# Kernel optimization log

Measured on AMD Instinct MI355X. Metric: run time of the kernel, lower is better.

The kernel has to match this reference:

```python
import jax, jax.numpy as jnp
import numpy as np

N = 50000
E = 800000
HID = 128


def _gat_conv(x, src, dst, W, al, ar, b, n):
    # DGL GATConv, num_heads=1, negative_slope=0.2, bias=True
    z = x @ W                                  # [N, F]
    el = z @ al                                # [N]
    er = z @ ar                                # [N]
    e = jax.nn.leaky_relu(el[src] + er[dst], 0.2)   # [E]
    m = jax.ops.segment_max(e, dst, num_segments=n)  # per-dst max for stable softmax
    ex = jnp.exp(e - m[dst])
    denom = jax.ops.segment_sum(ex, dst, num_segments=n)
    alpha = ex / (denom[dst] + 1e-9)           # edge softmax over incoming edges
    out = jax.ops.segment_sum(alpha[:, None] * z[src], dst, num_segments=n)
    return out + b


def setup_inputs() -> dict:
    key = jax.random.key(0)
    ks = jax.random.split(key, 16)
    inp = {
        "x": jax.random.normal(ks[0], (N, 2), jnp.float32),
        "src": jax.random.randint(ks[1], (E,), 0, N, jnp.int32),
        "dst": jax.random.randint(ks[2], (E,), 0, N, jnp.int32),
        "W1": jax.random.normal(ks[3], (2, HID), jnp.float32) * 0.5,
        "al1": jax.random.normal(ks[4], (HID,), jnp.float32) * 0.1,
        "ar1": jax.random.normal(ks[5], (HID,), jnp.float32) * 0.1,
        "b1": jnp.zeros((HID,), jnp.float32),
        "W2": jax.random.normal(ks[6], (HID, HID), jnp.float32) * (1.0 / np.sqrt(HID)),
        "al2": jax.random.normal(ks[7], (HID,), jnp.float32) * 0.1,
        "ar2": jax.random.normal(ks[8], (HID,), jnp.float32) * 0.1,
        "b2": jnp.zeros((HID,), jnp.float32),
        "Wlin": jax.random.normal(ks[9], (HID, 3), jnp.float32) * (1.0 / np.sqrt(HID)),
        "blin": jnp.zeros((3,), jnp.float32),
        "alpha0": jnp.float32(1.0),
        "beta0": jnp.float32(1.0),
        "gamma0": jnp.float32(1.0),
        "dt": jnp.float32(0.5),
    }
    return inp


def reference(x, src, dst, W1, al1, ar1, b1, W2, al2, ar2, b2, Wlin, blin,
              alpha0, beta0, gamma0, dt):
    h = _gat_conv(x, src, dst, W1, al1, ar1, b1, N)
    h = jax.nn.relu(h)
    h = _gat_conv(h, src, dst, W2, al2, ar2, b2, N)
    h = jax.nn.relu(h)
    h = jax.nn.sigmoid(h @ Wlin + blin)        # [N, 3]
    # (original computes unsplice/splice predictions from alpha0/beta0/gamma0/dt
    #  but does not return them; returned value is the mean over rate channels)
    return h.mean(axis=-1)                     # [N]


if __name__ == "__main__":
    out = reference(**setup_inputs())
    print(out.shape, out.dtype)
```

## Files before the change

### kernel.cpp

```cpp
#include <hip/hip_runtime.h>
#include <math.h>

#define NN 50000
#define EE 800000
#define HIDF 128
#define NPAD 50176

#define BSHIFT 9
#define BKTN 98
#define BCAP 10000

typedef unsigned int uint;
typedef unsigned short ushort;
typedef unsigned char uchar;
typedef short bf16x8 __attribute__((ext_vector_type(8)));
typedef float f32x4 __attribute__((ext_vector_type(4)));
typedef float f32x2 __attribute__((ext_vector_type(2)));

__device__ inline ushort bf16_rtne(float x) {
  uint u = __float_as_uint(x);
  return (ushort)((u + 0x7fffu + ((u >> 16) & 1u)) >> 16);
}
__device__ inline uint pack2_bf16(float a, float b) {
  return (uint)bf16_rtne(a) | ((uint)bf16_rtne(b) << 16);
}
__device__ inline float rdlanef(float p, int jj) {
  return __uint_as_float(__builtin_amdgcn_readlane(__float_as_uint(p), jj));
}
__device__ inline float lo16(uint z) { return __uint_as_float(z << 16); }
__device__ inline float hi16(uint z) { return __uint_as_float(z & 0xffff0000u); }

__global__ void k_prep(const float* __restrict__ x, const float* __restrict__ W1,
                       const float* __restrict__ al1, const float* __restrict__ ar1,
                       const float* __restrict__ W2, const float* __restrict__ al2,
                       const float* __restrict__ ar2,
                       ushort* __restrict__ z, float* __restrict__ el, float* __restrict__ er,
                       ushort* __restrict__ Bfrag, float* __restrict__ wel,
                       float* __restrict__ wer, int* __restrict__ bcnt) {
  int b = blockIdx.x, tid = threadIdx.x;
  if (b < 16) {
    int e = b * 1024 + tid * 4;
#pragma unroll
    for (int q = 0; q < 4; ++q, ++e) {
      int k = e >> 7, n = e & 127;
      float v = W2[e];
      ushort hi = bf16_rtne(v);
      ushort lo = bf16_rtne(v - __uint_as_float((uint)hi << 16));
      int g = n >> 4, t = k >> 5;
      int l = (n & 15) | (((k >> 3) & 3) << 4);
      int j = k & 7;
      int idx = ((g * 4 + t) * 64 + l) * 8 + j;
      Bfrag[idx] = hi;
      Bfrag[16384 + idx] = lo;
    }
  } else if (b == 16) {
    if (tid < BKTN) bcnt[tid] = 0;
    if (tid < 128) {
      float acc = 0.f;
      for (int k = 0; k < 128; ++k) acc += W2[k * 128 + tid] * al2[k];
      wel[tid] = acc;
    } else {
      int n = tid - 128;
      float acc = 0.f;
      for (int k = 0; k < 128; ++k) acc += W2[k * 128 + n] * ar2[k];
      wer[n] = acc;
    }
  } else {
    int v = (b - 17) * 4 + (tid >> 6);
    if (v >= NN) return;
    int lane = tid & 63;
    float x0 = x[v * 2 + 0];
    float x1 = x[v * 2 + 1];
    int f0 = lane * 2, f1 = f0 + 1;
    float z0 = fmaf(x0, W1[f0], x1 * W1[HIDF + f0]);
    float z1v = fmaf(x0, W1[f1], x1 * W1[HIDF + f1]);
    ((uint*)(z + (size_t)v * HIDF))[lane] = pack2_bf16(z0, z1v);
    float elp = z0 * al1[f0] + z1v * al1[f1];
    float erp = z0 * ar1[f0] + z1v * ar1[f1];
    for (int o = 32; o; o >>= 1) {
      elp += __shfl_xor(elp, o);
      erp += __shfl_xor(erp, o);
    }
    if (lane == 0) { el[v] = elp; er[v] = erp; }
  }
}

__global__ __launch_bounds__(256) void k_binA(const int* __restrict__ src,
                                              const int* __restrict__ dst,
                                              int* __restrict__ bcnt, uint* __restrict__ bcoo) {
  __shared__ uint stage[4096];
  __shared__ uchar stageb[4096];
  __shared__ int bh[BKTN], bbase[BKTN], gbase[BKTN], lcur[BKTN];
  __shared__ int sc[128];
  int tid = threadIdx.x;
  int e0 = blockIdx.x * 4096;
  int nE = min(4096, EE - e0);
  if (tid < BKTN) bh[tid] = 0;
  __syncthreads();

  int myb[16];
  uint myv[16];
#pragma unroll
  for (int k = 0; k < 16; ++k) {
    int i = e0 + k * 256 + tid;
    myb[k] = -1;
    if (i < EE) {
      int s = src[i], d = dst[i];
      myb[k] = d >> BSHIFT;
      myv[k] = ((uint)s << BSHIFT) | (uint)(d & 511);
      atomicAdd(&bh[myb[k]], 1);
    }
  }
  __syncthreads();

  {
    int v = (tid < BKTN) ? bh[tid] : 0;
    if (tid < 128) sc[tid] = v;
    __syncthreads();
    for (int o = 1; o < 128; o <<= 1) {
      int add = (tid >= o && tid < 128) ? sc[tid - o] : 0;
      __syncthreads();
      if (tid < 128) sc[tid] += add;
      __syncthreads();
    }
    if (tid < BKTN) {
      int excl = sc[tid] - bh[tid];
      bbase[tid] = excl;
      lcur[tid] = excl;
      gbase[tid] = atomicAdd(&bcnt[tid], bh[tid]);
    }
  }
  __syncthreads();

#pragma unroll
  for (int k = 0; k < 16; ++k) {
    if (myb[k] >= 0) {
      int slot = atomicAdd(&lcur[myb[k]], 1);
      stage[slot] = myv[k];
      stageb[slot] = (uchar)myb[k];
    }
  }
  __syncthreads();

  for (int s2 = tid; s2 < nE; s2 += 256) {
    int b = stageb[s2];
    bcoo[(size_t)b * BCAP + gbase[b] + (s2 - bbase[b])] = stage[s2];
  }
}

__global__ __launch_bounds__(256) void k_binB(const uint* __restrict__ bcoo,
                                              const int* __restrict__ bcnt,
                                              int* __restrict__ rowp, int* __restrict__ srcs) {
  __shared__ int h[512], pref[512], ps[256];
  __shared__ int basebuf;
  int b = blockIdx.x, tid = threadIdx.x;
  int cnt = bcnt[b];

  {
    int v = (tid < BKTN) ? bcnt[tid] : 0;
    if (tid < 128) ps[tid] = v;
    __syncthreads();
    for (int o = 1; o < 128; o <<= 1) {
      int add = (tid >= o && tid < 128) ? ps[tid - o] : 0;
      __syncthreads();
      if (tid < 128) ps[tid] += add;
      __syncthreads();
    }
    if (tid == 0) {
      basebuf = (b == 0) ? 0 : ps[b - 1];
      if (b == 0) rowp[NN] = EE;
    }
  }
  h[tid] = 0;
  h[tid + 256] = 0;
  __syncthreads();
  int base = basebuf;
  const uint* mc = bcoo + (size_t)b * BCAP;
  for (int i = tid; i < cnt; i += 256) atomicAdd(&h[mc[i] & 511], 1);
  __syncthreads();
  int a0 = h[2 * tid], a1 = h[2 * tid + 1];
  int s = a0 + a1;
  ps[tid] = s;
  __syncthreads();
  for (int o = 1; o < 256; o <<= 1) {
    int add = (tid >= o) ? ps[tid - o] : 0;
    __syncthreads();
    ps[tid] += add;
    __syncthreads();
  }
  int excl = ps[tid] - s;
  pref[2 * tid] = excl;
  pref[2 * tid + 1] = excl + a0;
  __syncthreads();
  int n0 = b << BSHIFT;
  for (int j = tid; j < 512; j += 256)
    if (n0 + j < NN) rowp[n0 + j] = base + pref[j];
  __syncthreads();
  for (int i = tid; i < cnt; i += 256) {
    uint v = mc[i];
    int pos = atomicAdd(&pref[v & 511], 1);
    srcs[base + pos] = (int)(v >> BSHIFT);
  }
}

__global__ __launch_bounds__(256) void k_gemm_mfma(
    const ushort* __restrict__ Hhi, const ushort* __restrict__ Hlo,
    const ushort* __restrict__ Bfrag, ushort* __restrict__ z) {
  int tid = threadIdx.x;
  int lane = tid & 63;
  int wid = tid >> 6;
  int base = blockIdx.x * 128;

  bf16x8 bhi[2][4], blo[2][4];
  const bf16x8* bp = (const bf16x8*)Bfrag;
#pragma unroll
  for (int gi = 0; gi < 2; ++gi)
#pragma unroll
    for (int t = 0; t < 4; ++t) {
      int idx = ((wid * 2 + gi) * 4 + t) * 64 + lane;
      bhi[gi][t] = bp[idx];
      blo[gi][t] = bp[2048 + idx];
    }

  int arow = lane & 15;
  int koff = (lane >> 4) * 8;
  const bf16x8* ahp = (const bf16x8*)(Hhi + (size_t)(base + arow) * HIDF + koff);
  const bf16x8* alp = (const bf16x8*)(Hlo + (size_t)(base + arow) * HIDF + koff);

  bf16x8 ah[4], av[4];
#pragma unroll
  for (int t = 0; t < 4; ++t) { ah[t] = ahp[t * 4]; av[t] = alp[t * 4]; }

#pragma unroll
  for (int mt = 0; mt < 8; ++mt) {
    bf16x8 nah[4], nav[4];
#pragma unroll
    for (int t = 0; t < 4; ++t) { nah[t] = ah[t]; nav[t] = av[t]; }
    if (mt < 7) {
#pragma unroll
      for (int t = 0; t < 4; ++t) {
        nah[t] = ahp[(mt + 1) * 256 + t * 4];
        nav[t] = alp[(mt + 1) * 256 + t * 4];
      }
    }
    f32x4 c0a = {0.f, 0.f, 0.f, 0.f}, c0b = {0.f, 0.f, 0.f, 0.f};
    f32x4 c1a = {0.f, 0.f, 0.f, 0.f}, c1b = {0.f, 0.f, 0.f, 0.f};
#pragma unroll
    for (int t = 0; t < 4; ++t) {
      f32x4& c0 = (t & 1) ? c0b : c0a;
      f32x4& c1 = (t & 1) ? c1b : c1a;
      c0 = __builtin_amdgcn_mfma_f32_16x16x32_bf16(ah[t], bhi[0][t], c0, 0, 0, 0);
      c1 = __builtin_amdgcn_mfma_f32_16x16x32_bf16(ah[t], bhi[1][t], c1, 0, 0, 0);
      c0 = __builtin_amdgcn_mfma_f32_16x16x32_bf16(ah[t], blo[0][t], c0, 0, 0, 0);
      c1 = __builtin_amdgcn_mfma_f32_16x16x32_bf16(ah[t], blo[1][t], c1, 0, 0, 0);
      c0 = __builtin_amdgcn_mfma_f32_16x16x32_bf16(av[t], bhi[0][t], c0, 0, 0, 0);
      c1 = __builtin_amdgcn_mfma_f32_16x16x32_bf16(av[t], bhi[1][t], c1, 0, 0, 0);
    }
    f32x4 c0 = c0a + c0b;
    f32x4 c1 = c1a + c1b;
    int r0 = base + mt * 16 + (lane >> 4) * 4;
    int cc = wid * 32 + (lane & 15);
    ushort* zp = z + (size_t)r0 * HIDF + cc;
#pragma unroll
    for (int i = 0; i < 4; ++i) {
      zp[i * HIDF] = bf16_rtne(c0[i]);
      zp[i * HIDF + 16] = bf16_rtne(c1[i]);
    }
#pragma unroll
    for (int t = 0; t < 4; ++t) { ah[t] = nah[t]; av[t] = nav[t]; }
  }
}

#define PAIR(JJ)                                                        \
  {                                                                     \
    float pA = rdlanef(p, (JJ)), pB = rdlanef(p, (JJ) + 1);             \
    int sA = __builtin_amdgcn_readlane(s, (JJ));                        \
    int sB = __builtin_amdgcn_readlane(s, (JJ) + 1);                    \
    uint zA = zl[(uint)sA * 64u];                                       \
    uint zB = zl[(uint)sB * 64u];                                       \
    f32x2 vA = {lo16(zA), hi16(zA)};                                    \
    f32x2 vB = {lo16(zB), hi16(zB)};                                    \
    acc = vA * (f32x2){pA, pA} + acc;                                   \
    acc = vB * (f32x2){pB, pB} + acc;                                   \
  }

template <int MODE>
__global__ void k_aggregate(const int* __restrict__ rowp, const int* __restrict__ srcs,
                            const float* __restrict__ el, const float* __restrict__ er,
                            const ushort* __restrict__ z, const float* __restrict__ bias,
                            ushort* __restrict__ Hhi, ushort* __restrict__ Hlo,
                            const float* __restrict__ wel, const float* __restrict__ wer,
                            float* __restrict__ elo, float* __restrict__ ero,
                            float* __restrict__ out,
                            const float* __restrict__ Wlin, const float* __restrict__ blin) {
  int v = blockIdx.x * 4 + (threadIdx.x >> 6);
  if (v >= NN) return;
  int lane = threadIdx.x & 63;
  int beg = rowp[v], end = rowp[v + 1];
  float erv = er[v];
  float psum = 0.f;
  f32x2 acc = {0.f, 0.f};
  const uint* zl = (const uint*)z + lane;

  for (int cb = beg; cb < end; cb += 64) {
    int j = cb + lane;
    int s = srcs[min(j, end - 1)];
    float t = el[s] + erv;
    t = fmaxf(t, 0.2f * t);
    float p = (j < end) ? __expf(t) : 0.f;
    psum += p;
    int cnt = min(64, end - cb);
    int bb = 0;
    for (; bb + 16 <= cnt; bb += 16) {
#pragma unroll
      for (int u = 0; u < 16; u += 2) PAIR(bb + u)
    }
    for (; bb < cnt; bb += 2) PAIR(bb)
  }

  float denom = psum;
  for (int o = 32; o; o >>= 1) denom += __shfl_xor(denom, o);
  float inv = 1.0f / (denom + 1e-9f);
  float2 bv = ((const float2*)bias)[lane];
  float ox = fmaxf(fmaf(acc.x, inv, bv.x), 0.f);
  float oy = fmaxf(fmaf(acc.y, inv, bv.y), 0.f);

  if (MODE == 1) {
    ushort hx = bf16_rtne(ox), hy = bf16_rtne(oy);
    ((uint*)Hhi)[(size_t)v * 64 + lane] = (uint)hx | ((uint)hy << 16);
    float lx = ox - __uint_as_float((uint)hx << 16);
    float ly = oy - __uint_as_float((uint)hy << 16);
    ((uint*)Hlo)[(size_t)v * 64 + lane] = pack2_bf16(lx, ly);
    float2 wl = ((const float2*)wel)[lane];
    float2 wr = ((const float2*)wer)[lane];
    float ep = ox * wl.x + oy * wl.y;
    float rp = ox * wr.x + oy * wr.y;
    for (int o = 32; o; o >>= 1) {
      ep += __shfl_xor(ep, o);
      rp += __shfl_xor(rp, o);
    }
    if (lane == 0) { elo[v] = ep; ero[v] = rp; }
  } else {
    int f0 = lane * 2;
    const float* w0 = &Wlin[f0 * 3];
    float d0 = fmaf(ox, w0[0], oy * w0[3]);
    float d1 = fmaf(ox, w0[1], oy * w0[4]);
    float d2 = fmaf(ox, w0[2], oy * w0[5]);
    for (int o = 32; o; o >>= 1) {
      d0 += __shfl_xor(d0, o);
      d1 += __shfl_xor(d1, o);
      d2 += __shfl_xor(d2, o);
    }
    if (lane == 0) {
      float s0 = 1.f / (1.f + __expf(-(d0 + blin[0])));
      float s1 = 1.f / (1.f + __expf(-(d1 + blin[1])));
      float s2 = 1.f / (1.f + __expf(-(d2 + blin[2])));
      out[v] = (s0 + s1 + s2) * (1.f / 3.f);
    }
  }
}

extern "C" void kernel_launch(void* const* d_in, const int* in_sizes, int n_in,
                              void* d_out, int out_size, void* d_ws, size_t ws_size,
                              hipStream_t stream) {
  const float* x    = (const float*)d_in[0];
  const int*   src  = (const int*)d_in[1];
  const int*   dst  = (const int*)d_in[2];
  const float* W1   = (const float*)d_in[3];
  const float* al1  = (const float*)d_in[4];
  const float* ar1  = (const float*)d_in[5];
  const float* b1   = (const float*)d_in[6];
  const float* W2   = (const float*)d_in[7];
  const float* al2  = (const float*)d_in[8];
  const float* ar2  = (const float*)d_in[9];
  const float* b2   = (const float*)d_in[10];
  const float* Wlin = (const float*)d_in[11];
  const float* blin = (const float*)d_in[12];
  float* out = (float*)d_out;

  char* ws = (char*)d_ws;
  size_t off = 0;
  auto alloc = [&](size_t bytes) -> char* {
    char* p = ws + off;
    off += (bytes + 255) & ~(size_t)255;
    return p;
  };
  int*    rowp    = (int*)alloc((size_t)(NN + 1) * 4);
  int*    srcs    = (int*)alloc((size_t)EE * 4);
  int*    bcnt    = (int*)alloc(BKTN * 4);
  uint*   bcoo    = (uint*)alloc((size_t)BKTN * BCAP * 4);
  float*  el1     = (float*)alloc((size_t)NN * 4);
  float*  er1     = (float*)alloc((size_t)NN * 4);
  float*  el2     = (float*)alloc((size_t)NN * 4);
  float*  er2     = (float*)alloc((size_t)NN * 4);
  float*  wel     = (float*)alloc(HIDF * 4);
  float*  wer     = (float*)alloc(HIDF * 4);
  ushort* Bfrag   = (ushort*)alloc(2 * 16384 * 2);
  ushort* Z       = (ushort*)alloc((size_t)NPAD * HIDF * 2);
  ushort* Hhi     = (ushort*)alloc((size_t)NPAD * HIDF * 2);
  ushort* Hlo     = (ushort*)alloc((size_t)NPAD * HIDF * 2);

  const int nbNode4 = (NN + 3) / 4;
  const int nbGemm = (NN + 127) / 128;
  const int nbBinA = (EE + 4095) / 4096;

  k_prep<<<17 + nbNode4, 256, 0, stream>>>(x, W1, al1, ar1, W2, al2, ar2,
                                           Z, el1, er1, Bfrag, wel, wer, bcnt);

  k_binA<<<nbBinA, 256, 0, stream>>>(src, dst, bcnt, bcoo);
  k_binB<<<BKTN, 256, 0, stream>>>(bcoo, bcnt, rowp, srcs);

  k_aggregate<1><<<nbNode4, 256, 0, stream>>>(rowp, srcs, el1, er1, Z, b1,
                                              Hhi, Hlo, wel, wer, el2, er2,
                                              nullptr, nullptr, nullptr);

  k_gemm_mfma<<<nbGemm, 256, 0, stream>>>(Hhi, Hlo, Bfrag, Z);
  k_aggregate<2><<<nbNode4, 256, 0, stream>>>(rowp, srcs, el2, er2, Z, b2,
                                              nullptr, nullptr, nullptr, nullptr, nullptr, nullptr,
                                              out, Wlin, blin);
}
```

Before: 146.5 us.

## Aggregate layer-1 in 2-D input space instead of 128-wide features

Because layer 1 is linear with a 2-wide input, the attention logits are now computed as x·(W1·al1) and x·(W1·ar1). The softmax-weighted sum aggregates the 2-float x rows rather than the 128-wide bf16 z rows, and W1 and the bias are applied per destination node afterwards. This removes the per-node z/el/er materialisation in k_prep and the 128-feature gather per edge in layer 1. The aggregation is also done per-lane rather than by broadcasting each edge across the wave. The result is now kept in fp32 where it was previously rounded to bf16 z, and the summation order changes.

```diff
diff --git a/kernel.cpp b/kernel.cpp
--- a/kernel.cpp
+++ b/kernel.cpp
@@ -30,13 +30,13 @@
 __device__ inline float lo16(uint z) { return __uint_as_float(z << 16); }
 __device__ inline float hi16(uint z) { return __uint_as_float(z & 0xffff0000u); }
 
-__global__ void k_prep(const float* __restrict__ x, const float* __restrict__ W1,
-                       const float* __restrict__ al1, const float* __restrict__ ar1,
+__global__ void k_prep(const float* __restrict__ W1, const float* __restrict__ al1,
+                       const float* __restrict__ ar1,
                        const float* __restrict__ W2, const float* __restrict__ al2,
                        const float* __restrict__ ar2,
-                       ushort* __restrict__ z, float* __restrict__ el, float* __restrict__ er,
                        ushort* __restrict__ Bfrag, float* __restrict__ wel,
-                       float* __restrict__ wer, int* __restrict__ bcnt) {
+                       float* __restrict__ wer, float* __restrict__ params,
+                       int* __restrict__ bcnt) {
   int b = blockIdx.x, tid = threadIdx.x;
   if (b < 16) {
     int e = b * 1024 + tid * 4;
@@ -53,7 +53,7 @@
       Bfrag[idx] = hi;
       Bfrag[16384 + idx] = lo;
     }
-  } else if (b == 16) {
+  } else {
     if (tid < BKTN) bcnt[tid] = 0;
     if (tid < 128) {
       float acc = 0.f;
@@ -65,23 +65,13 @@
       for (int k = 0; k < 128; ++k) acc += W2[k * 128 + n] * ar2[k];
       wer[n] = acc;
     }
-  } else {
-    int v = (b - 17) * 4 + (tid >> 6);
-    if (v >= NN) return;
-    int lane = tid & 63;
-    float x0 = x[v * 2 + 0];
-    float x1 = x[v * 2 + 1];
-    int f0 = lane * 2, f1 = f0 + 1;
-    float z0 = fmaf(x0, W1[f0], x1 * W1[HIDF + f0]);
-    float z1v = fmaf(x0, W1[f1], x1 * W1[HIDF + f1]);
-    ((uint*)(z + (size_t)v * HIDF))[lane] = pack2_bf16(z0, z1v);
-    float elp = z0 * al1[f0] + z1v * al1[f1];
-    float erp = z0 * ar1[f0] + z1v * ar1[f1];
-    for (int o = 32; o; o >>= 1) {
-      elp += __shfl_xor(elp, o);
-      erp += __shfl_xor(erp, o);
-    }
-    if (lane == 0) { el[v] = elp; er[v] = erp; }
+    if (tid < 4) {
+      const float* vec = (tid & 2) ? ar1 : al1;
+      const float* wrow = W1 + (tid & 1) * HIDF;
+      float acc = 0.f;
+      for (int f = 0; f < HIDF; ++f) acc += wrow[f] * vec[f];
+      params[tid] = acc;
+    }
   }
 }
 
@@ -203,6 +193,62 @@
   }
 }
 
+__global__ void k_agg1(const int* __restrict__ rowp, const int* __restrict__ srcs,
+                       const float* __restrict__ x, const float* __restrict__ params,
+                       const float* __restrict__ W1, const float* __restrict__ b1,
+                       ushort* __restrict__ Hhi, ushort* __restrict__ Hlo,
+                       const float* __restrict__ wel, const float* __restrict__ wer,
+                       float* __restrict__ el2, float* __restrict__ er2) {
+  int v = blockIdx.x * 4 + (threadIdx.x >> 6);
+  if (v >= NN) return;
+  int lane = threadIdx.x & 63;
+  float wl1x = params[0], wl1y = params[1], wr1x = params[2], wr1y = params[3];
+  float2 xv = ((const float2*)x)[v];
+  float erv = fmaf(xv.x, wr1x, xv.y * wr1y);
+  int beg = rowp[v], end = rowp[v + 1];
+
+  float psum = 0.f, ax = 0.f, ay = 0.f;
+  for (int j = beg + lane; j < end; j += 64) {
+    int s = srcs[j];
+    float2 xs = ((const float2*)x)[s];
+    float t = fmaf(xs.x, wl1x, xs.y * wl1y) + erv;
+    t = fmaxf(t, 0.2f * t);
+    float p = __expf(t);
+    psum += p;
+    ax = fmaf(p, xs.x, ax);
+    ay = fmaf(p, xs.y, ay);
+  }
+  for (int o = 32; o; o >>= 1) {
+    psum += __shfl_xor(psum, o);
+    ax += __shfl_xor(ax, o);
+    ay += __shfl_xor(ay, o);
+  }
+  float inv = 1.0f / (psum + 1e-9f);
+  ax *= inv;
+  ay *= inv;
+
+  float2 w0 = ((const float2*)W1)[lane];
+  float2 w1 = ((const float2*)(W1 + HIDF))[lane];
+  float2 bv = ((const float2*)b1)[lane];
+  float ox = fmaxf(fmaf(ax, w0.x, fmaf(ay, w1.x, bv.x)), 0.f);
+  float oy = fmaxf(fmaf(ax, w0.y, fmaf(ay, w1.y, bv.y)), 0.f);
+
+  ushort hx = bf16_rtne(ox), hy = bf16_rtne(oy);
+  ((uint*)Hhi)[(size_t)v * 64 + lane] = (uint)hx | ((uint)hy << 16);
+  float lx = ox - __uint_as_float((uint)hx << 16);
+  float ly = oy - __uint_as_float((uint)hy << 16);
+  ((uint*)Hlo)[(size_t)v * 64 + lane] = pack2_bf16(lx, ly);
+  float2 wl = ((const float2*)wel)[lane];
+  float2 wr = ((const float2*)wer)[lane];
+  float ep = ox * wl.x + oy * wl.y;
+  float rp = ox * wr.x + oy * wr.y;
+  for (int o = 32; o; o >>= 1) {
+    ep += __shfl_xor(ep, o);
+    rp += __shfl_xor(rp, o);
+  }
+  if (lane == 0) { el2[v] = ep; er2[v] = rp; }
+}
+
 __global__ __launch_bounds__(256) void k_gemm_mfma(
     const ushort* __restrict__ Hhi, const ushort* __restrict__ Hlo,
     const ushort* __restrict__ Bfrag, ushort* __restrict__ z) {
@@ -284,15 +330,11 @@
     acc = vB * (f32x2){pB, pB} + acc;                                   \
   }
 
-template <int MODE>
-__global__ void k_aggregate(const int* __restrict__ rowp, const int* __restrict__ srcs,
-                            const float* __restrict__ el, const float* __restrict__ er,
-                            const ushort* __restrict__ z, const float* __restrict__ bias,
-                            ushort* __restrict__ Hhi, ushort* __restrict__ Hlo,
-                            const float* __restrict__ wel, const float* __restrict__ wer,
-                            float* __restrict__ elo, float* __restrict__ ero,
-                            float* __restrict__ out,
-                            const float* __restrict__ Wlin, const float* __restrict__ blin) {
+__global__ void k_agg2(const int* __restrict__ rowp, const int* __restrict__ srcs,
+                       const float* __restrict__ el, const float* __restrict__ er,
+                       const ushort* __restrict__ z, const float* __restrict__ bias,
+                       float* __restrict__ out,
+                       const float* __restrict__ Wlin, const float* __restrict__ blin) {
   int v = blockIdx.x * 4 + (threadIdx.x >> 6);
   if (v >= NN) return;
   int lane = threadIdx.x & 63;
@@ -325,38 +367,21 @@
   float ox = fmaxf(fmaf(acc.x, inv, bv.x), 0.f);
   float oy = fmaxf(fmaf(acc.y, inv, bv.y), 0.f);
 
-  if (MODE == 1) {
-    ushort hx = bf16_rtne(ox), hy = bf16_rtne(oy);
-    ((uint*)Hhi)[(size_t)v * 64 + lane] = (uint)hx | ((uint)hy << 16);
-    float lx = ox - __uint_as_float((uint)hx << 16);
-    float ly = oy - __uint_as_float((uint)hy << 16);
-    ((uint*)Hlo)[(size_t)v * 64 + lane] = pack2_bf16(lx, ly);
-    float2 wl = ((const float2*)wel)[lane];
-    float2 wr = ((const float2*)wer)[lane];
-    float ep = ox * wl.x + oy * wl.y;
-    float rp = ox * wr.x + oy * wr.y;
-    for (int o = 32; o; o >>= 1) {
-      ep += __shfl_xor(ep, o);
-      rp += __shfl_xor(rp, o);
-    }
-    if (lane == 0) { elo[v] = ep; ero[v] = rp; }
-  } else {
-    int f0 = lane * 2;
-    const float* w0 = &Wlin[f0 * 3];
-    float d0 = fmaf(ox, w0[0], oy * w0[3]);
-    float d1 = fmaf(ox, w0[1], oy * w0[4]);
-    float d2 = fmaf(ox, w0[2], oy * w0[5]);
-    for (int o = 32; o; o >>= 1) {
-      d0 += __shfl_xor(d0, o);
-      d1 += __shfl_xor(d1, o);
-      d2 += __shfl_xor(d2, o);
-    }
-    if (lane == 0) {
-      float s0 = 1.f / (1.f + __expf(-(d0 + blin[0])));
-      float s1 = 1.f / (1.f + __expf(-(d1 + blin[1])));
-      float s2 = 1.f / (1.f + __expf(-(d2 + blin[2])));
-      out[v] = (s0 + s1 + s2) * (1.f / 3.f);
-    }
+  int f0 = lane * 2;
+  const float* w0 = &Wlin[f0 * 3];
+  float d0 = fmaf(ox, w0[0], oy * w0[3]);
+  float d1 = fmaf(ox, w0[1], oy * w0[4]);
+  float d2 = fmaf(ox, w0[2], oy * w0[5]);
+  for (int o = 32; o; o >>= 1) {
+    d0 += __shfl_xor(d0, o);
+    d1 += __shfl_xor(d1, o);
+    d2 += __shfl_xor(d2, o);
+  }
+  if (lane == 0) {
+    float s0 = 1.f / (1.f + __expf(-(d0 + blin[0])));
+    float s1 = 1.f / (1.f + __expf(-(d1 + blin[1])));
+    float s2 = 1.f / (1.f + __expf(-(d2 + blin[2])));
+    out[v] = (s0 + s1 + s2) * (1.f / 3.f);
   }
 }
 
@@ -385,37 +410,33 @@
     off += (bytes + 255) & ~(size_t)255;
     return p;
   };
-  int*    rowp    = (int*)alloc((size_t)(NN + 1) * 4);
-  int*    srcs    = (int*)alloc((size_t)EE * 4);
-  int*    bcnt    = (int*)alloc(BKTN * 4);
-  uint*   bcoo    = (uint*)alloc((size_t)BKTN * BCAP * 4);
-  float*  el1     = (float*)alloc((size_t)NN * 4);
-  float*  er1     = (float*)alloc((size_t)NN * 4);
-  float*  el2     = (float*)alloc((size_t)NN * 4);
-  float*  er2     = (float*)alloc((size_t)NN * 4);
-  float*  wel     = (float*)alloc(HIDF * 4);
-  float*  wer     = (float*)alloc(HIDF * 4);
-  ushort* Bfrag   = (ushort*)alloc(2 * 16384 * 2);
-  ushort* Z       = (ushort*)alloc((size_t)NPAD * HIDF * 2);
-  ushort* Hhi     = (ushort*)alloc((size_t)NPAD * HIDF * 2);
-  ushort* Hlo     = (ushort*)alloc((size_t)NPAD * HIDF * 2);
+  int*    rowp   = (int*)alloc((size_t)(NN + 1) * 4);
+  int*    srcs   = (int*)alloc((size_t)EE * 4);
+  int*    bcnt   = (int*)alloc(BKTN * 4);
+  uint*   bcoo   = (uint*)alloc((size_t)BKTN * BCAP * 4);
+  float*  el2    = (float*)alloc((size_t)NN * 4);
+  float*  er2    = (float*)alloc((size_t)NN * 4);
+  float*  wel    = (float*)alloc(HIDF * 4);
+  float*  wer    = (float*)alloc(HIDF * 4);
+  float*  params = (float*)alloc(16 * 4);
+  ushort* Bfrag  = (ushort*)alloc(2 * 16384 * 2);
+  ushort* Z      = (ushort*)alloc((size_t)NPAD * HIDF * 2);
+  ushort* Hhi    = (ushort*)alloc((size_t)NPAD * HIDF * 2);
+  ushort* Hlo    = (ushort*)alloc((size_t)NPAD * HIDF * 2);
 
   const int nbNode4 = (NN + 3) / 4;
   const int nbGemm = (NN + 127) / 128;
   const int nbBinA = (EE + 4095) / 4096;
 
-  k_prep<<<17 + nbNode4, 256, 0, stream>>>(x, W1, al1, ar1, W2, al2, ar2,
-                                           Z, el1, er1, Bfrag, wel, wer, bcnt);
+  k_prep<<<17, 256, 0, stream>>>(W1, al1, ar1, W2, al2, ar2,
+                                 Bfrag, wel, wer, params, bcnt);
 
   k_binA<<<nbBinA, 256, 0, stream>>>(src, dst, bcnt, bcoo);
   k_binB<<<BKTN, 256, 0, stream>>>(bcoo, bcnt, rowp, srcs);
 
-  k_aggregate<1><<<nbNode4, 256, 0, stream>>>(rowp, srcs, el1, er1, Z, b1,
-                                              Hhi, Hlo, wel, wer, el2, er2,
-                                              nullptr, nullptr, nullptr);
+  k_agg1<<<nbNode4, 256, 0, stream>>>(rowp, srcs, x, params, W1, b1,
+                                      Hhi, Hlo, wel, wer, el2, er2);
 
   k_gemm_mfma<<<nbGemm, 256, 0, stream>>>(Hhi, Hlo, Bfrag, Z);
-  k_aggregate<2><<<nbNode4, 256, 0, stream>>>(rowp, srcs, el2, er2, Z, b2,
-                                              nullptr, nullptr, nullptr, nullptr, nullptr, nullptr,
-                                              out, Wlin, blin);
-}
+  k_agg2<<<nbNode4, 256, 0, stream>>>(rowp, srcs, el2, er2, Z, b2, out, Wlin, blin);
+}
```

Measured after the change: 120.9 us (median of 2 runs). -17.5%, faster.
